# Optimization experiments

Hardware: AMD Instinct MI355X
Metric: run time of the kernel (lower is better)

Reference implementation:

```python
import jax, jax.numpy as jnp
import numpy as np

B, S, T, E, D = 16, 2048, 1024, 256, 256  # batch, src_len, tgt_len, enc_size, dec_size


def setup_inputs() -> dict:
    key = jax.random.key(0)
    k1, k2, k3, k4, k5 = jax.random.split(key, 5)
    enc_states = jax.random.normal(k1, (B, S, E), dtype=jnp.float32)
    dec_states = jax.random.normal(k2, (B, T, D), dtype=jnp.float32)
    # valid-prefix mask: each row has at least one valid (True) source position
    lengths = jax.random.randint(k3, (B,), 1, S + 1)
    src_mask = jnp.arange(S)[None, :] < lengths[:, None]  # (B, S) bool
    # Dense layer weights (no bias). Glorot-ish scale.
    W_enc = jax.random.normal(k4, (E, D), dtype=jnp.float32) / np.sqrt(E)
    W_fin = jax.random.normal(k5, (E + D, D), dtype=jnp.float32) / np.sqrt(E + D)
    return {"enc_states": enc_states, "dec_states": dec_states,
            "src_mask": src_mask, "W_enc": W_enc, "W_fin": W_fin}


def reference(enc_states, dec_states, src_mask, W_enc, W_fin):
    # enc_trnsfrmr: (B,S,E) @ (E,D) -> (B,S,D)
    enc_proj = jnp.einsum('bse,ed->bsd', enc_states, W_enc)
    # attention scores: batch_dot(dec_states, enc_proj^T) -> (B,T,S)
    scores = jnp.einsum('btd,bsd->bts', dec_states, enc_proj)
    scores = jnp.where(src_mask[:, None, :], scores, -jnp.inf)
    wts = jax.nn.softmax(scores, axis=-1)  # (B,T,S)
    # broadcast-multiply + reduce_sum == weighted sum over src positions
    context = jnp.einsum('bts,bse->bte', wts, enc_states)  # (B,T,E)
    cat = jnp.concatenate([context, dec_states], axis=-1)  # (B,T,E+D)
    return jnp.tanh(jnp.einsum('btf,fd->btd', cat, W_fin))  # (B,T,D)
```

## Files before the change

### kernel.cpp

```cpp
#include <hip/hip_runtime.h>
#include <math.h>
#include <stdint.h>

#define NB 16
#define NS 2048
#define NT 1024
#define NE 256
#define ND 256
#define NM (NB * NT)

typedef short sh8 __attribute__((ext_vector_type(8)));
typedef float f4v __attribute__((ext_vector_type(4)));

static __device__ __forceinline__ float bf2f(unsigned short u) {
    union { unsigned int i; float f; } v;
    v.i = ((unsigned int)u) << 16;
    return v.f;
}
static __device__ __forceinline__ unsigned short f2bf(float f) {
    union { unsigned int i; float f; } v;
    v.f = f;
    unsigned int x = v.i;
    x += 0x7FFFu + ((x >> 16) & 1u);
    return (unsigned short)(x >> 16);
}
static __device__ __forceinline__ float4 load4(const void* p, int isbf, long idx) {
    if (isbf) {
        const unsigned short* h = (const unsigned short*)p + idx;
        ushort4 u = *(const ushort4*)h;
        return make_float4(bf2f(u.x), bf2f(u.y), bf2f(u.z), bf2f(u.w));
    }
    const float* f = (const float*)p + idx;
    return *(const float4*)f;
}
static __device__ __forceinline__ int mvalid(const void* m, int kind, int b, int s) {
    long idx = (long)b * NS + s;
    switch (kind) {
        case 0:  return ((const unsigned char*)m)[idx] != 0;
        case 1:  return ((const int*)m)[idx] != 0;
        case 2:  return ((const unsigned short*)m)[idx] != 0;
        default: return ((const unsigned int*)m)[idx] != 0;
    }
}

__global__ void k_detect(const void* __restrict__ enc_raw,
                         const void* __restrict__ mask_raw,
                         int* __restrict__ flags) {
    __shared__ int cnt;
    if (threadIdx.x == 0) cnt = 0;
    __syncthreads();
    const unsigned short* h = (const unsigned short*)enc_raw;
    int local = 0;
    for (int i = threadIdx.x; i < 4096; i += 256) {
        int ex = (h[i] >> 7) & 0xFF;
        if (ex >= 97 && ex <= 157) local++;
    }
    atomicAdd(&cnt, local);
    __syncthreads();
    if (threadIdx.x == 0) {
        int isbf = (cnt >= 3700) ? 1 : 0;
        const unsigned char* mb = (const unsigned char*)mask_raw;
        int kind;
        if (mb[1] == 0x3F)                       kind = 2;
        else if (mb[3] == 0x3F && mb[1] == 0)    kind = 3;
        else if (mb[1] == 1)                     kind = 0;
        else if (mb[4] == 1 || mb[8] == 1)       kind = 1;
        else                                     kind = (mb[NS] == 1) ? 0 : 1;
        flags[0] = isbf;
        flags[1] = kind;
    }
}

__global__ __launch_bounds__(256) void k_split_e(const void* __restrict__ enc,
                                                 const int* __restrict__ flags,
                                                 unsigned short* __restrict__ eh,
                                                 unsigned short* __restrict__ el) {
    const int isbf = flags[0];
    const long i = ((long)blockIdx.x * 256 + threadIdx.x) * 8;
    if (isbf) {
        sh8 v = *(const sh8*)((const unsigned short*)enc + i);
        *(sh8*)(eh + i) = v;
    } else {
        const float* f = (const float*)enc + i;
        sh8 hv, lv;
#pragma unroll
        for (int j = 0; j < 8; ++j) {
            float x = f[j];
            unsigned short h = f2bf(x);
            hv[j] = (short)h;
            lv[j] = (short)f2bf(x - bf2f(h));
        }
        *(sh8*)(eh + i) = hv;
        *(sh8*)(el + i) = lv;
    }
}

__global__ __launch_bounds__(256) void k_q(const void* __restrict__ dec,
                                           const void* __restrict__ Wenc,
                                           const int* __restrict__ flags,
                                           unsigned short* __restrict__ qh,
                                           unsigned short* __restrict__ ql) {
    const int isbf = flags[0];
    const int tid = threadIdx.x;
    const int tx = tid & 15, ty = tid >> 4;
    const int m0 = blockIdx.x * 64, n0 = blockIdx.y * 64;
    __shared__ float As[16][68];
    __shared__ float Bs[16][68];
    float acc[4][4] = {};
    const int lrow = tid >> 2;
    const int lk4  = (tid & 3) << 2;
    for (int kt = 0; kt < ND; kt += 16) {
        float4 av = load4(dec,  isbf, (long)(m0 + lrow) * ND + kt + lk4);
        float4 bv = load4(Wenc, isbf, (long)(n0 + lrow) * ND + kt + lk4);
        As[lk4 + 0][lrow] = av.x; As[lk4 + 1][lrow] = av.y;
        As[lk4 + 2][lrow] = av.z; As[lk4 + 3][lrow] = av.w;
        Bs[lk4 + 0][lrow] = bv.x; Bs[lk4 + 1][lrow] = bv.y;
        Bs[lk4 + 2][lrow] = bv.z; Bs[lk4 + 3][lrow] = bv.w;
        __syncthreads();
#pragma unroll
        for (int k = 0; k < 16; ++k) {
            float4 a = *(const float4*)&As[k][ty << 2];
            float4 b = *(const float4*)&Bs[k][tx << 2];
            acc[0][0] = fmaf(a.x, b.x, acc[0][0]); acc[0][1] = fmaf(a.x, b.y, acc[0][1]);
            acc[0][2] = fmaf(a.x, b.z, acc[0][2]); acc[0][3] = fmaf(a.x, b.w, acc[0][3]);
            acc[1][0] = fmaf(a.y, b.x, acc[1][0]); acc[1][1] = fmaf(a.y, b.y, acc[1][1]);
            acc[1][2] = fmaf(a.y, b.z, acc[1][2]); acc[1][3] = fmaf(a.y, b.w, acc[1][3]);
            acc[2][0] = fmaf(a.z, b.x, acc[2][0]); acc[2][1] = fmaf(a.z, b.y, acc[2][1]);
            acc[2][2] = fmaf(a.z, b.z, acc[2][2]); acc[2][3] = fmaf(a.z, b.w, acc[2][3]);
            acc[3][0] = fmaf(a.w, b.x, acc[3][0]); acc[3][1] = fmaf(a.w, b.y, acc[3][1]);
            acc[3][2] = fmaf(a.w, b.z, acc[3][2]); acc[3][3] = fmaf(a.w, b.w, acc[3][3]);
        }
        __syncthreads();
    }
#pragma unroll
    for (int i = 0; i < 4; ++i) {
        long base = (long)(m0 + (ty << 2) + i) * NE + n0 + (tx << 2);
        ushort4 hv, lv;
        {
            float f0 = acc[i][0]; unsigned short h = f2bf(f0); hv.x = h; lv.x = f2bf(f0 - bf2f(h));
            float f1 = acc[i][1]; h = f2bf(f1); hv.y = h; lv.y = f2bf(f1 - bf2f(h));
            float f2 = acc[i][2]; h = f2bf(f2); hv.z = h; lv.z = f2bf(f2 - bf2f(h));
            float f3 = acc[i][3]; h = f2bf(f3); hv.w = h; lv.w = f2bf(f3 - bf2f(h));
        }
        *(ushort4*)&qh[base] = hv;
        *(ushort4*)&ql[base] = lv;
    }
}

__global__ __launch_bounds__(256, 2) void k_attn(
    const unsigned short* __restrict__ qh, const unsigned short* __restrict__ ql,
    const unsigned short* __restrict__ eh, const unsigned short* __restrict__ el,
    const void* __restrict__ mask, const int* __restrict__ flags,
    float* __restrict__ ctx, float* __restrict__ Mp, float* __restrict__ Lp)
{
    const int isbf  = flags[0];
    const int mkind = flags[1];
    const int b  = blockIdx.y;
    const int t0 = blockIdx.x * 32;
    const int part = blockIdx.z, nparts = gridDim.z;
    const int tid  = threadIdx.x;
    const int lane = tid & 63;
    const int wid  = tid >> 6;
    const int th = wid & 1;
    const int sh = wid >> 1;
    const int lr = lane & 15;
    const int lg = lane >> 4;

    __shared__ __align__(16) unsigned short EHR[32][264];
    __shared__ __align__(16) unsigned short ELR[32][264];
    __shared__ __align__(16) unsigned short VT[2][256][40];
    __shared__ __align__(16) float PBs[32][36];
    __shared__ float hm[2][32];
    __shared__ float hs[2][32];
    __shared__ int s_len;

    if (tid == 0) s_len = 0;
    __syncthreads();
    {
        int c = 0;
#pragma unroll
        for (int j = 0; j < 8; ++j) c += mvalid(mask, mkind, b, tid * 8 + j);
        atomicAdd(&s_len, c);
    }
    __syncthreads();
    const int len  = s_len;
    const int s_lo = part * (NS / nparts);
    const int s_hi = min(s_lo + NS / nparts, len);
    const int ntiles = (s_hi > s_lo) ? ((s_hi - s_lo + 31) >> 5) : 0;
    const long mrow = (long)part * NM + (long)b * NT + t0;
    if (ntiles == 0) {
        if (nparts > 1 && tid < 32) { Mp[mrow + tid] = -INFINITY; Lp[mrow + tid] = 0.f; }
        return;
    }

    sh8 qhf[8], qlf[8];
    {
        const unsigned short* qp  = qh + ((long)b * NT + t0 + th * 16 + lr) * NE + lg * 8;
        const unsigned short* qp2 = ql + ((long)b * NT + t0 + th * 16 + lr) * NE + lg * 8;
#pragma unroll
        for (int k8 = 0; k8 < 8; ++k8) {
            qhf[k8] = *(const sh8*)(qp  + k8 * 32);
            qlf[k8] = *(const sh8*)(qp2 + k8 * 32);
        }
    }

    f4v O[8];
#pragma unroll
    for (int et = 0; et < 8; ++et) O[et] = (f4v){0.f, 0.f, 0.f, 0.f};
    float Mreg4[4], L4[4], MregP = -INFINITY;
#pragma unroll
    for (int r = 0; r < 4; ++r) { Mreg4[r] = -INFINITY; L4[r] = 0.f; }

    const int ss = tid >> 3;
    const int ee = (tid & 7) * 8;
    const int swzw = ((tid & 7) & 3) << 3;

    sh8 rh[4], rl[4];
    {
        const unsigned short* eg = eh + ((long)b * NS + s_lo + ss) * NE;
#pragma unroll
        for (int c = 0; c < 4; ++c) rh[c] = *(const sh8*)(eg + ee + c * 64);
        if (!isbf) {
            const unsigned short* eg2 = el + ((long)b * NS + s_lo + ss) * NE;
#pragma unroll
            for (int c = 0; c < 4; ++c) rl[c] = *(const sh8*)(eg2 + ee + c * 64);
        }
#pragma unroll
        for (int c = 0; c < 4; ++c) {
            const int e0 = ee + c * 64;
            *(sh8*)&EHR[ss][e0] = rh[c];
            if (!isbf) *(sh8*)&ELR[ss][e0] = rl[c];
            const int cs = ss ^ swzw;
#pragma unroll
            for (int j = 0; j < 8; ++j) VT[0][e0 + j][cs] = (unsigned short)rh[c][j];
        }
    }
    int cur = 0;

    for (int it = 0; it < ntiles; ++it) {
        const int s0 = s_lo + it * 32;
        __syncthreads();
        f4v cacc = (f4v){0.f, 0.f, 0.f, 0.f};
        {
            const unsigned short* ep = &EHR[sh * 16 + lr][lg * 8];
            const unsigned short* lp = &ELR[sh * 16 + lr][lg * 8];
            if (isbf) {
#pragma unroll
                for (int k8 = 0; k8 < 8; ++k8) {
                    sh8 ea = *(const sh8*)(ep + k8 * 32);
                    cacc = __builtin_amdgcn_mfma_f32_16x16x32_bf16(ea, qhf[k8], cacc, 0, 0, 0);
                    cacc = __builtin_amdgcn_mfma_f32_16x16x32_bf16(ea, qlf[k8], cacc, 0, 0, 0);
                }
            } else {
#pragma unroll
                for (int k8 = 0; k8 < 8; ++k8) {
                    sh8 ea = *(const sh8*)(ep + k8 * 32);
                    sh8 eb = *(const sh8*)(lp + k8 * 32);
                    cacc = __builtin_amdgcn_mfma_f32_16x16x32_bf16(ea, qhf[k8], cacc, 0, 0, 0);
                    cacc = __builtin_amdgcn_mfma_f32_16x16x32_bf16(ea, qlf[k8], cacc, 0, 0, 0);
                    cacc = __builtin_amdgcn_mfma_f32_16x16x32_bf16(eb, qhf[k8], cacc, 0, 0, 0);
                }
            }
        }
        float sc[4];
#pragma unroll
        for (int r = 0; r < 4; ++r) {
            int sl = sh * 16 + lg * 4 + r;
            sc[r] = (s0 + sl < len) ? cacc[r] : -INFINITY;
        }
        float m4 = fmaxf(fmaxf(sc[0], sc[1]), fmaxf(sc[2], sc[3]));
        m4 = fmaxf(m4, __shfl_xor(m4, 16));
        m4 = fmaxf(m4, __shfl_xor(m4, 32));
        float p[4], ps = 0.f;
#pragma unroll
        for (int r = 0; r < 4; ++r) {
            p[r] = (sc[r] == -INFINITY) ? 0.f : __expf(sc[r] - m4);
            ps += p[r];
        }
        ps += __shfl_xor(ps, 16);
        ps += __shfl_xor(ps, 32);
        if (lane < 16) { hm[sh][th * 16 + lane] = m4; hs[sh][th * 16 + lane] = ps; }
        *(float4*)&PBs[th * 16 + lr][sh * 16 + lg * 4] = make_float4(p[0], p[1], p[2], p[3]);
        __syncthreads();
        float f0, f1, al[4];
        {
            const int tP = th * 16 + lr;
            float h0 = hm[0][tP], h1 = hm[1][tP];
            float Mn = fmaxf(MregP, fmaxf(h0, h1));
            f0 = __expf(h0 - Mn);
            f1 = __expf(h1 - Mn);
            MregP = Mn;
        }
#pragma unroll
        for (int r = 0; r < 4; ++r) {
            const int t4 = th * 16 + lg * 4 + r;
            float g0 = hm[0][t4], g1 = hm[1][t4];
            float Mn = fmaxf(Mreg4[r], fmaxf(g0, g1));
            al[r] = __expf(Mreg4[r] - Mn);
            L4[r] = L4[r] * al[r] + hs[0][t4] * __expf(g0 - Mn) + hs[1][t4] * __expf(g1 - Mn);
            Mreg4[r] = Mn;
        }
        const int more = (it + 1 < ntiles);
        if (more) {
            const unsigned short* eg = eh + ((long)b * NS + s0 + 32 + ss) * NE;
#pragma unroll
            for (int c = 0; c < 4; ++c) rh[c] = *(const sh8*)(eg + ee + c * 64);
            if (!isbf) {
                const unsigned short* eg2 = el + ((long)b * NS + s0 + 32 + ss) * NE;
#pragma unroll
                for (int c = 0; c < 4; ++c) rl[c] = *(const sh8*)(eg2 + ee + c * 64);
            }
        }
        {
            const float fsc = (lg < 2) ? f0 : f1;
            f4v pA = *(const f4v*)&PBs[th * 16 + lr][lg * 8];
            f4v pB = *(const f4v*)&PBs[th * 16 + lr][lg * 8 + 4];
            sh8 pf;
#pragma unroll
            for (int j = 0; j < 4; ++j) {
                pf[j]     = (short)f2bf(pA[j] * fsc);
                pf[4 + j] = (short)f2bf(pB[j] * fsc);
            }
            f4v alv = (f4v){al[0], al[1], al[2], al[3]};
#pragma unroll
            for (int et = 0; et < 8; ++et) O[et] *= alv;
#pragma unroll
            for (int et = 0; et < 8; ++et) {
                const int row = sh * 128 + et * 16 + lr;
                sh8 vf = *(const sh8*)&VT[cur][row][(lg ^ ((row >> 3) & 3)) * 8];
                O[et] = __builtin_amdgcn_mfma_f32_16x16x32_bf16(pf, vf, O[et], 0, 0, 0);
            }
        }
        if (more) {
#pragma unroll
            for (int c = 0; c < 4; ++c) {
                const int e0 = ee + c * 64;
                *(sh8*)&EHR[ss][e0] = rh[c];
                if (!isbf) *(sh8*)&ELR[ss][e0] = rl[c];
                const int cs = ss ^ swzw;
#pragma unroll
                for (int j = 0; j < 8; ++j) VT[cur ^ 1][e0 + j][cs] = (unsigned short)rh[c][j];
            }
            cur ^= 1;
        }
    }
    if (nparts == 1) {
        f4v inv;
#pragma unroll
        for (int r = 0; r < 4; ++r) inv[r] = 1.0f / L4[r];
#pragma unroll
        for (int et = 0; et < 8; ++et) {
            f4v ov = O[et] * inv;
            long rbase = ((long)b * NT + t0 + th * 16 + lg * 4) * NE + sh * 128 + et * 16 + lr;
#pragma unroll
            for (int r = 0; r < 4; ++r)
                ctx[rbase + (long)r * NE] = ov[r];
        }
    } else {
        float* op = ctx + (long)part * NM * NE;
#pragma unroll
        for (int et = 0; et < 8; ++et) {
            long rbase = ((long)b * NT + t0 + th * 16 + lg * 4) * NE + sh * 128 + et * 16 + lr;
#pragma unroll
            for (int r = 0; r < 4; ++r)
                op[rbase + (long)r * NE] = O[et][r];
        }
        if (sh == 0 && lr == 0) {
#pragma unroll
            for (int r = 0; r < 4; ++r) {
                Mp[mrow + th * 16 + lg * 4 + r] = Mreg4[r];
                Lp[mrow + th * 16 + lg * 4 + r] = L4[r];
            }
        }
    }
}

__global__ __launch_bounds__(256) void k_comb(float* __restrict__ ctx,
                                              const float* __restrict__ Mp,
                                              const float* __restrict__ Lp,
                                              int nparts) {
    const long m = (long)blockIdx.x * 8 + (threadIdx.x >> 5);
    const int  e0 = (threadIdx.x & 31) * 8;
    float Mv[4], Lv[4];
    float M = -INFINITY;
    for (int p = 0; p < nparts; ++p) {
        Mv[p] = Mp[(long)p * NM + m];
        Lv[p] = Lp[(long)p * NM + m];
        if (Lv[p] > 0.f) M = fmaxf(M, Mv[p]);
    }
    float L = 0.f, w[4];
    for (int p = 0; p < nparts; ++p) {
        w[p] = (Lv[p] > 0.f) ? __expf(Mv[p] - M) : 0.f;
        L += Lv[p] * w[p];
    }
    float o[8] = {};
    for (int p = 0; p < nparts; ++p) {
        if (w[p] > 0.f) {
            const float* src = ctx + (long)p * NM * NE + m * NE + e0;
            f4v a = *(const f4v*)src;
            f4v c = *(const f4v*)(src + 4);
#pragma unroll
            for (int j = 0; j < 4; ++j) { o[j] += a[j] * w[p]; o[4 + j] += c[j] * w[p]; }
        }
    }
    const float inv = 1.0f / L;
    float* dst = ctx + m * NE + e0;
    f4v r0, r1;
#pragma unroll
    for (int j = 0; j < 4; ++j) { r0[j] = o[j] * inv; r1[j] = o[4 + j] * inv; }
    *(f4v*)dst = r0;
    *(f4v*)(dst + 4) = r1;
}

__global__ __launch_bounds__(256) void k_final(const float* __restrict__ ctx,
                                               const void* __restrict__ dec,
                                               const void* __restrict__ Wfin,
                                               const int* __restrict__ flags,
                                               void* __restrict__ out) {
    const int isbf = flags[0];
    const int tid = threadIdx.x;
    const int tx = tid & 15, ty = tid >> 4;
    const int m0 = blockIdx.x * 64, n0 = blockIdx.y * 64;
    __shared__ float As[16][68];
    __shared__ float Bs[16][68];
    float acc[4][4] = {};
    const int lrow = tid >> 2;
    const int lk4  = (tid & 3) << 2;
    const int lkb  = tid >> 4;
    const int ln4  = (tid & 15) << 2;
    for (int kt = 0; kt < NE + ND; kt += 16) {
        float4 av;
        if (kt < NE) {
            av = *(const float4*)&ctx[(long)(m0 + lrow) * NE + kt + lk4];
        } else {
            av = load4(dec, isbf, (long)(m0 + lrow) * ND + (kt - NE) + lk4);
        }
        float4 bv = load4(Wfin, isbf, (long)(kt + lkb) * ND + n0 + ln4);
        As[lk4 + 0][lrow] = av.x; As[lk4 + 1][lrow] = av.y;
        As[lk4 + 2][lrow] = av.z; As[lk4 + 3][lrow] = av.w;
        *(float4*)&Bs[lkb][ln4] = bv;
        __syncthreads();
#pragma unroll
        for (int k = 0; k < 16; ++k) {
            float4 a = *(const float4*)&As[k][ty << 2];
            float4 b = *(const float4*)&Bs[k][tx << 2];
            acc[0][0] = fmaf(a.x, b.x, acc[0][0]); acc[0][1] = fmaf(a.x, b.y, acc[0][1]);
            acc[0][2] = fmaf(a.x, b.z, acc[0][2]); acc[0][3] = fmaf(a.x, b.w, acc[0][3]);
            acc[1][0] = fmaf(a.y, b.x, acc[1][0]); acc[1][1] = fmaf(a.y, b.y, acc[1][1]);
            acc[1][2] = fmaf(a.y, b.z, acc[1][2]); acc[1][3] = fmaf(a.y, b.w, acc[1][3]);
            acc[2][0] = fmaf(a.z, b.x, acc[2][0]); acc[2][1] = fmaf(a.z, b.y, acc[2][1]);
            acc[2][2] = fmaf(a.z, b.z, acc[2][2]); acc[2][3] = fmaf(a.z, b.w, acc[2][3]);
            acc[3][0] = fmaf(a.w, b.x, acc[3][0]); acc[3][1] = fmaf(a.w, b.y, acc[3][1]);
            acc[3][2] = fmaf(a.w, b.z, acc[3][2]); acc[3][3] = fmaf(a.w, b.w, acc[3][3]);
        }
        __syncthreads();
    }
    if (isbf) {
        unsigned short* o = (unsigned short*)out;
#pragma unroll
        for (int i = 0; i < 4; ++i) {
            long base = (long)(m0 + (ty << 2) + i) * ND + n0 + (tx << 2);
            ushort4 r;
            r.x = f2bf(tanhf(acc[i][0])); r.y = f2bf(tanhf(acc[i][1]));
            r.z = f2bf(tanhf(acc[i][2])); r.w = f2bf(tanhf(acc[i][3]));
            *(ushort4*)&o[base] = r;
        }
    } else {
        float* o = (float*)out;
#pragma unroll
        for (int i = 0; i < 4; ++i) {
            long base = (long)(m0 + (ty << 2) + i) * ND + n0 + (tx << 2);
            float4 r = make_float4(tanhf(acc[i][0]), tanhf(acc[i][1]),
                                   tanhf(acc[i][2]), tanhf(acc[i][3]));
            *(float4*)&o[base] = r;
        }
    }
}

extern "C" void kernel_launch(void* const* d_in, const int* in_sizes, int n_in,
                              void* d_out, int out_size, void* d_ws, size_t ws_size,
                              hipStream_t stream) {
    const void* enc  = d_in[0];
    const void* dec  = d_in[1];
    const void* mask = d_in[2];
    const void* Wenc = d_in[3];
    const void* Wfin = d_in[4];

    unsigned short* ehb = (unsigned short*)d_ws;
    unsigned short* elb = ehb + (size_t)NB * NS * NE;
    unsigned short* qhb = elb + (size_t)NB * NS * NE;
    unsigned short* qlb = qhb + (size_t)NM * NE;
    const size_t fixed = ((size_t)NB * NS * NE * 2 + (size_t)NM * NE * 2) * 2;

    int parts = 1;
    for (int p = 4; p >= 1; p >>= 1) {
        size_t need = fixed + (size_t)p * NM * NE * 4 + (size_t)p * NM * 8 + 256;
        if (ws_size >= need) { parts = p; break; }
    }
    float* ctx  = (float*)(qlb + (size_t)NM * NE);
    float* Mpb  = ctx + (size_t)parts * NM * NE;
    float* Lpb  = Mpb + (size_t)parts * NM;
    int*   flags = (int*)(Lpb + (size_t)parts * NM);

    k_detect<<<1, 256, 0, stream>>>(enc, mask, flags);
    k_split_e<<<(NB * NS * NE) / (256 * 8), 256, 0, stream>>>(enc, flags, ehb, elb);
    k_q<<<dim3(NM / 64, NE / 64), 256, 0, stream>>>(dec, Wenc, flags, qhb, qlb);
    k_attn<<<dim3(NT / 32, NB, parts), 256, 0, stream>>>(qhb, qlb, ehb, elb, mask, flags,
                                                         ctx, Mpb, Lpb);
    if (parts > 1)
        k_comb<<<NM / 8, 256, 0, stream>>>(ctx, Mpb, Lpb, parts);
    k_final<<<dim3(NM / 64, ND / 64), 256, 0, stream>>>(ctx, dec, Wfin, flags, d_out);
}
```

Before: 315.7 us.

## Move query and final projections to split-bf16 MFMA GEMMs

Replaces the FP32 SIMT tiled GEMMs for the query projection and the final concatenated projection with MFMA kernels using hi/lo bf16 splitting (three products) to keep near-FP32 accuracy. Adds split kernels for dec, W_enc and a transposed W_fin. The attention and combine kernels now emit context as hi/lo bf16, reusing the query buffers, so the final GEMM reads MFMA-ready operands. This trades extra preprocessing launches and memory traffic for much higher matrix throughput, and aliasing the q buffers as outputs requires dropping restrict.

```diff
diff --git a/kernel.cpp b/kernel.cpp
--- a/kernel.cpp
+++ b/kernel.cpp
@@ -8,6 +8,7 @@
 #define NE 256
 #define ND 256
 #define NM (NB * NT)
+#define KF (NE + ND)
 
 typedef short sh8 __attribute__((ext_vector_type(8)));
 typedef float f4v __attribute__((ext_vector_type(4)));
@@ -71,17 +72,17 @@
     }
 }
 
-__global__ __launch_bounds__(256) void k_split_e(const void* __restrict__ enc,
-                                                 const int* __restrict__ flags,
-                                                 unsigned short* __restrict__ eh,
-                                                 unsigned short* __restrict__ el) {
+__global__ __launch_bounds__(256) void k_split(const void* __restrict__ src,
+                                               const int* __restrict__ flags,
+                                               unsigned short* __restrict__ hh,
+                                               unsigned short* __restrict__ ll) {
     const int isbf = flags[0];
     const long i = ((long)blockIdx.x * 256 + threadIdx.x) * 8;
     if (isbf) {
-        sh8 v = *(const sh8*)((const unsigned short*)enc + i);
-        *(sh8*)(eh + i) = v;
+        sh8 v = *(const sh8*)((const unsigned short*)src + i);
+        *(sh8*)(hh + i) = v;
     } else {
-        const float* f = (const float*)enc + i;
+        const float* f = (const float*)src + i;
         sh8 hv, lv;
 #pragma unroll
         for (int j = 0; j < 8; ++j) {
@@ -90,68 +91,124 @@
             hv[j] = (short)h;
             lv[j] = (short)f2bf(x - bf2f(h));
         }
-        *(sh8*)(eh + i) = hv;
-        *(sh8*)(el + i) = lv;
-    }
-}
-
-__global__ __launch_bounds__(256) void k_q(const void* __restrict__ dec,
-                                           const void* __restrict__ Wenc,
-                                           const int* __restrict__ flags,
-                                           unsigned short* __restrict__ qh,
-                                           unsigned short* __restrict__ ql) {
+        *(sh8*)(hh + i) = hv;
+        *(sh8*)(ll + i) = lv;
+    }
+}
+
+__global__ __launch_bounds__(256) void k_twf(const void* __restrict__ Wfin,
+                                             const int* __restrict__ flags,
+                                             unsigned short* __restrict__ wfh,
+                                             unsigned short* __restrict__ wfl) {
     const int isbf = flags[0];
+    __shared__ float T[64][68];
+    const int f0 = blockIdx.x * 64, n0 = blockIdx.y * 64;
     const int tid = threadIdx.x;
-    const int tx = tid & 15, ty = tid >> 4;
-    const int m0 = blockIdx.x * 64, n0 = blockIdx.y * 64;
-    __shared__ float As[16][68];
-    __shared__ float Bs[16][68];
-    float acc[4][4] = {};
-    const int lrow = tid >> 2;
-    const int lk4  = (tid & 3) << 2;
-    for (int kt = 0; kt < ND; kt += 16) {
-        float4 av = load4(dec,  isbf, (long)(m0 + lrow) * ND + kt + lk4);
-        float4 bv = load4(Wenc, isbf, (long)(n0 + lrow) * ND + kt + lk4);
-        As[lk4 + 0][lrow] = av.x; As[lk4 + 1][lrow] = av.y;
-        As[lk4 + 2][lrow] = av.z; As[lk4 + 3][lrow] = av.w;
-        Bs[lk4 + 0][lrow] = bv.x; Bs[lk4 + 1][lrow] = bv.y;
-        Bs[lk4 + 2][lrow] = bv.z; Bs[lk4 + 3][lrow] = bv.w;
-        __syncthreads();
-#pragma unroll
-        for (int k = 0; k < 16; ++k) {
-            float4 a = *(const float4*)&As[k][ty << 2];
-            float4 b = *(const float4*)&Bs[k][tx << 2];
-            acc[0][0] = fmaf(a.x, b.x, acc[0][0]); acc[0][1] = fmaf(a.x, b.y, acc[0][1]);
-            acc[0][2] = fmaf(a.x, b.z, acc[0][2]); acc[0][3] = fmaf(a.x, b.w, acc[0][3]);
-            acc[1][0] = fmaf(a.y, b.x, acc[1][0]); acc[1][1] = fmaf(a.y, b.y, acc[1][1]);
-            acc[1][2] = fmaf(a.y, b.z, acc[1][2]); acc[1][3] = fmaf(a.y, b.w, acc[1][3]);
-            acc[2][0] = fmaf(a.z, b.x, acc[2][0]); acc[2][1] = fmaf(a.z, b.y, acc[2][1]);
-            acc[2][2] = fmaf(a.z, b.z, acc[2][2]); acc[2][3] = fmaf(a.z, b.w, acc[2][3]);
-            acc[3][0] = fmaf(a.w, b.x, acc[3][0]); acc[3][1] = fmaf(a.w, b.y, acc[3][1]);
-            acc[3][2] = fmaf(a.w, b.z, acc[3][2]); acc[3][3] = fmaf(a.w, b.w, acc[3][3]);
-        }
-        __syncthreads();
-    }
 #pragma unroll
     for (int i = 0; i < 4; ++i) {
-        long base = (long)(m0 + (ty << 2) + i) * NE + n0 + (tx << 2);
+        int idx = tid + i * 256;
+        int r = idx >> 4, c4 = (idx & 15) << 2;
+        float4 v = load4(Wfin, isbf, (long)(f0 + r) * ND + n0 + c4);
+        T[r][c4] = v.x; T[r][c4 + 1] = v.y; T[r][c4 + 2] = v.z; T[r][c4 + 3] = v.w;
+    }
+    __syncthreads();
+#pragma unroll
+    for (int i = 0; i < 4; ++i) {
+        int idx = tid + i * 256;
+        int n = idx >> 4, f4 = (idx & 15) << 2;
         ushort4 hv, lv;
-        {
-            float f0 = acc[i][0]; unsigned short h = f2bf(f0); hv.x = h; lv.x = f2bf(f0 - bf2f(h));
-            float f1 = acc[i][1]; h = f2bf(f1); hv.y = h; lv.y = f2bf(f1 - bf2f(h));
-            float f2 = acc[i][2]; h = f2bf(f2); hv.z = h; lv.z = f2bf(f2 - bf2f(h));
-            float f3 = acc[i][3]; h = f2bf(f3); hv.w = h; lv.w = f2bf(f3 - bf2f(h));
-        }
-        *(ushort4*)&qh[base] = hv;
-        *(ushort4*)&ql[base] = lv;
-    }
+        float x;
+        x = T[f4 + 0][n]; hv.x = f2bf(x); lv.x = f2bf(x - bf2f(hv.x));
+        x = T[f4 + 1][n]; hv.y = f2bf(x); lv.y = f2bf(x - bf2f(hv.y));
+        x = T[f4 + 2][n]; hv.z = f2bf(x); lv.z = f2bf(x - bf2f(hv.z));
+        x = T[f4 + 3][n]; hv.w = f2bf(x); lv.w = f2bf(x - bf2f(hv.w));
+        long base = (long)(n0 + n) * KF + f0 + f4;
+        *(ushort4*)&wfh[base] = hv;
+        *(ushort4*)&wfl[base] = lv;
+    }
+}
+
+__global__ __launch_bounds__(256) void k_q_m(const unsigned short* __restrict__ dh,
+                                             const unsigned short* __restrict__ dl,
+                                             const unsigned short* __restrict__ wh,
+                                             const unsigned short* __restrict__ wl,
+                                             const int* __restrict__ flags,
+                                             unsigned short* __restrict__ qh,
+                                             unsigned short* __restrict__ ql) {
+    const int isbf = flags[0];
+    const int lane = threadIdx.x & 63, wid = threadIdx.x >> 6;
+    const int lr = lane & 15, lg = lane >> 4;
+    const long m0 = (long)blockIdx.x * 64 + (wid & 1) * 32;
+    const int  n0 = blockIdx.y * 64 + (wid >> 1) * 32;
+    const unsigned short* Ah = dh + (m0 + lr) * ND + lg * 8;
+    const unsigned short* Al = dl + (m0 + lr) * ND + lg * 8;
+    const unsigned short* Bh = wh + (long)(n0 + lr) * ND + lg * 8;
+    const unsigned short* Bl = wl + (long)(n0 + lr) * ND + lg * 8;
+    f4v acc[2][2];
+#pragma unroll
+    for (int i = 0; i < 2; ++i)
+#pragma unroll
+        for (int j = 0; j < 2; ++j) acc[i][j] = (f4v){0.f, 0.f, 0.f, 0.f};
+    if (isbf) {
+#pragma unroll
+        for (int k8 = 0; k8 < 8; ++k8) {
+            const int ko = k8 * 32;
+            sh8 a0 = *(const sh8*)(Ah + ko);
+            sh8 a1 = *(const sh8*)(Ah + 16 * ND + ko);
+            sh8 b0 = *(const sh8*)(Bh + ko);
+            sh8 b1 = *(const sh8*)(Bh + 16 * ND + ko);
+            acc[0][0] = __builtin_amdgcn_mfma_f32_16x16x32_bf16(a0, b0, acc[0][0], 0, 0, 0);
+            acc[0][1] = __builtin_amdgcn_mfma_f32_16x16x32_bf16(a0, b1, acc[0][1], 0, 0, 0);
+            acc[1][0] = __builtin_amdgcn_mfma_f32_16x16x32_bf16(a1, b0, acc[1][0], 0, 0, 0);
+            acc[1][1] = __builtin_amdgcn_mfma_f32_16x16x32_bf16(a1, b1, acc[1][1], 0, 0, 0);
+        }
+    } else {
+#pragma unroll
+        for (int k8 = 0; k8 < 8; ++k8) {
+            const int ko = k8 * 32;
+            sh8 a0 = *(const sh8*)(Ah + ko);
+            sh8 a1 = *(const sh8*)(Ah + 16 * ND + ko);
+            sh8 b0 = *(const sh8*)(Bh + ko);
+            sh8 b1 = *(const sh8*)(Bh + 16 * ND + ko);
+            sh8 la0 = *(const sh8*)(Al + ko);
+            sh8 la1 = *(const sh8*)(Al + 16 * ND + ko);
+            sh8 lb0 = *(const sh8*)(Bl + ko);
+            sh8 lb1 = *(const sh8*)(Bl + 16 * ND + ko);
+            acc[0][0] = __builtin_amdgcn_mfma_f32_16x16x32_bf16(a0, b0, acc[0][0], 0, 0, 0);
+            acc[0][0] = __builtin_amdgcn_mfma_f32_16x16x32_bf16(la0, b0, acc[0][0], 0, 0, 0);
+            acc[0][0] = __builtin_amdgcn_mfma_f32_16x16x32_bf16(a0, lb0, acc[0][0], 0, 0, 0);
+            acc[0][1] = __builtin_amdgcn_mfma_f32_16x16x32_bf16(a0, b1, acc[0][1], 0, 0, 0);
+            acc[0][1] = __builtin_amdgcn_mfma_f32_16x16x32_bf16(la0, b1, acc[0][1], 0, 0, 0);
+            acc[0][1] = __builtin_amdgcn_mfma_f32_16x16x32_bf16(a0, lb1, acc[0][1], 0, 0, 0);
+            acc[1][0] = __builtin_amdgcn_mfma_f32_16x16x32_bf16(a1, b0, acc[1][0], 0, 0, 0);
+            acc[1][0] = __builtin_amdgcn_mfma_f32_16x16x32_bf16(la1, b0, acc[1][0], 0, 0, 0);
+            acc[1][0] = __builtin_amdgcn_mfma_f32_16x16x32_bf16(a1, lb0, acc[1][0], 0, 0, 0);
+            acc[1][1] = __builtin_amdgcn_mfma_f32_16x16x32_bf16(a1, b1, acc[1][1], 0, 0, 0);
+            acc[1][1] = __builtin_amdgcn_mfma_f32_16x16x32_bf16(la1, b1, acc[1][1], 0, 0, 0);
+            acc[1][1] = __builtin_amdgcn_mfma_f32_16x16x32_bf16(a1, lb1, acc[1][1], 0, 0, 0);
+        }
+    }
+#pragma unroll
+    for (int mi = 0; mi < 2; ++mi)
+#pragma unroll
+        for (int r = 0; r < 4; ++r) {
+            long rowb = (m0 + mi * 16 + lg * 4 + r) * NE + n0 + lr;
+#pragma unroll
+            for (int ni = 0; ni < 2; ++ni) {
+                float v = acc[mi][ni][r];
+                unsigned short h = f2bf(v);
+                qh[rowb + ni * 16] = h;
+                ql[rowb + ni * 16] = f2bf(v - bf2f(h));
+            }
+        }
 }
 
 __global__ __launch_bounds__(256, 2) void k_attn(
-    const unsigned short* __restrict__ qh, const unsigned short* __restrict__ ql,
+    const unsigned short* qh, const unsigned short* ql,
     const unsigned short* __restrict__ eh, const unsigned short* __restrict__ el,
     const void* __restrict__ mask, const int* __restrict__ flags,
-    float* __restrict__ ctx, float* __restrict__ Mp, float* __restrict__ Lp)
+    unsigned short* ch, unsigned short* cl,
+    float* __restrict__ pctx, float* __restrict__ Mp, float* __restrict__ Lp)
 {
     const int isbf  = flags[0];
     const int mkind = flags[1];
@@ -353,11 +410,15 @@
             f4v ov = O[et] * inv;
             long rbase = ((long)b * NT + t0 + th * 16 + lg * 4) * NE + sh * 128 + et * 16 + lr;
 #pragma unroll
-            for (int r = 0; r < 4; ++r)
-                ctx[rbase + (long)r * NE] = ov[r];
+            for (int r = 0; r < 4; ++r) {
+                float v = ov[r];
+                unsigned short h = f2bf(v);
+                ch[rbase + (long)r * NE] = h;
+                cl[rbase + (long)r * NE] = f2bf(v - bf2f(h));
+            }
         }
     } else {
-        float* op = ctx + (long)part * NM * NE;
+        float* op = pctx + (long)part * NM * NE;
 #pragma unroll
         for (int et = 0; et < 8; ++et) {
             long rbase = ((long)b * NT + t0 + th * 16 + lg * 4) * NE + sh * 128 + et * 16 + lr;
@@ -375,10 +436,12 @@
     }
 }
 
-__global__ __launch_bounds__(256) void k_comb(float* __restrict__ ctx,
+__global__ __launch_bounds__(256) void k_comb(const float* __restrict__ pctx,
                                               const float* __restrict__ Mp,
                                               const float* __restrict__ Lp,
-                                              int nparts) {
+                                              int nparts,
+                                              unsigned short* __restrict__ ch,
+                                              unsigned short* __restrict__ cl) {
     const long m = (long)blockIdx.x * 8 + (threadIdx.x >> 5);
     const int  e0 = (threadIdx.x & 31) * 8;
     float Mv[4], Lv[4];
@@ -396,7 +459,7 @@
     float o[8] = {};
     for (int p = 0; p < nparts; ++p) {
         if (w[p] > 0.f) {
-            const float* src = ctx + (long)p * NM * NE + m * NE + e0;
+            const float* src = pctx + (long)p * NM * NE + m * NE + e0;
             f4v a = *(const f4v*)src;
             f4v c = *(const f4v*)(src + 4);
 #pragma unroll
@@ -404,76 +467,126 @@
         }
     }
     const float inv = 1.0f / L;
-    float* dst = ctx + m * NE + e0;
-    f4v r0, r1;
-#pragma unroll
-    for (int j = 0; j < 4; ++j) { r0[j] = o[j] * inv; r1[j] = o[4 + j] * inv; }
-    *(f4v*)dst = r0;
-    *(f4v*)(dst + 4) = r1;
-}
-
-__global__ __launch_bounds__(256) void k_final(const float* __restrict__ ctx,
-                                               const void* __restrict__ dec,
-                                               const void* __restrict__ Wfin,
+    unsigned short hv[8], lv[8];
+#pragma unroll
+    for (int j = 0; j < 8; ++j) {
+        float v = o[j] * inv;
+        unsigned short h = f2bf(v);
+        hv[j] = h;
+        lv[j] = f2bf(v - bf2f(h));
+    }
+    long base = m * NE + e0;
+    *(ushort4*)&ch[base]     = *(ushort4*)&hv[0];
+    *(ushort4*)&ch[base + 4] = *(ushort4*)&hv[4];
+    *(ushort4*)&cl[base]     = *(ushort4*)&lv[0];
+    *(ushort4*)&cl[base + 4] = *(ushort4*)&lv[4];
+}
+
+__global__ __launch_bounds__(256) void k_fin_m(const unsigned short* __restrict__ ch,
+                                               const unsigned short* __restrict__ cl,
+                                               const unsigned short* __restrict__ dh,
+                                               const unsigned short* __restrict__ dl,
+                                               const unsigned short* __restrict__ wh,
+                                               const unsigned short* __restrict__ wl,
                                                const int* __restrict__ flags,
                                                void* __restrict__ out) {
     const int isbf = flags[0];
-    const int tid = threadIdx.x;
-    const int tx = tid & 15, ty = tid >> 4;
-    const int m0 = blockIdx.x * 64, n0 = blockIdx.y * 64;
-    __shared__ float As[16][68];
-    __shared__ float Bs[16][68];
-    float acc[4][4] = {};
-    const int lrow = tid >> 2;
-    const int lk4  = (tid & 3) << 2;
-    const int lkb  = tid >> 4;
-    const int ln4  = (tid & 15) << 2;
-    for (int kt = 0; kt < NE + ND; kt += 16) {
-        float4 av;
-        if (kt < NE) {
-            av = *(const float4*)&ctx[(long)(m0 + lrow) * NE + kt + lk4];
-        } else {
-            av = load4(dec, isbf, (long)(m0 + lrow) * ND + (kt - NE) + lk4);
-        }
-        float4 bv = load4(Wfin, isbf, (long)(kt + lkb) * ND + n0 + ln4);
-        As[lk4 + 0][lrow] = av.x; As[lk4 + 1][lrow] = av.y;
-        As[lk4 + 2][lrow] = av.z; As[lk4 + 3][lrow] = av.w;
-        *(float4*)&Bs[lkb][ln4] = bv;
-        __syncthreads();
-#pragma unroll
-        for (int k = 0; k < 16; ++k) {
-            float4 a = *(const float4*)&As[k][ty << 2];
-            float4 b = *(const float4*)&Bs[k][tx << 2];
-            acc[0][0] = fmaf(a.x, b.x, acc[0][0]); acc[0][1] = fmaf(a.x, b.y, acc[0][1]);
-            acc[0][2] = fmaf(a.x, b.z, acc[0][2]); acc[0][3] = fmaf(a.x, b.w, acc[0][3]);
-            acc[1][0] = fmaf(a.y, b.x, acc[1][0]); acc[1][1] = fmaf(a.y, b.y, acc[1][1]);
-            acc[1][2] = fmaf(a.y, b.z, acc[1][2]); acc[1][3] = fmaf(a.y, b.w, acc[1][3]);
-            acc[2][0] = fmaf(a.z, b.x, acc[2][0]); acc[2][1] = fmaf(a.z, b.y, acc[2][1]);
-            acc[2][2] = fmaf(a.z, b.z, acc[2][2]); acc[2][3] = fmaf(a.z, b.w, acc[2][3]);
-            acc[3][0] = fmaf(a.w, b.x, acc[3][0]); acc[3][1] = fmaf(a.w, b.y, acc[3][1]);
-            acc[3][2] = fmaf(a.w, b.z, acc[3][2]); acc[3][3] = fmaf(a.w, b.w, acc[3][3]);
-        }
-        __syncthreads();
+    const int lane = threadIdx.x & 63, wid = threadIdx.x >> 6;
+    const int lr = lane & 15, lg = lane >> 4;
+    const long m0 = (long)blockIdx.x * 64 + (wid & 1) * 32;
+    const int  n0 = blockIdx.y * 64 + (wid >> 1) * 32;
+    const unsigned short* Bh = wh + (long)(n0 + lr) * KF + lg * 8;
+    const unsigned short* Bl = wl + (long)(n0 + lr) * KF + lg * 8;
+    f4v acc[2][2];
+#pragma unroll
+    for (int i = 0; i < 2; ++i)
+#pragma unroll
+        for (int j = 0; j < 2; ++j) acc[i][j] = (f4v){0.f, 0.f, 0.f, 0.f};
+
+    {
+        const unsigned short* Ah = ch + (m0 + lr) * NE + lg * 8;
+        const unsigned short* Al = cl + (m0 + lr) * NE + lg * 8;
+#pragma unroll
+        for (int k8 = 0; k8 < 8; ++k8) {
+            const int ko = k8 * 32;
+            sh8 a0 = *(const sh8*)(Ah + ko);
+            sh8 a1 = *(const sh8*)(Ah + 16 * NE + ko);
+            sh8 la0 = *(const sh8*)(Al + ko);
+            sh8 la1 = *(const sh8*)(Al + 16 * NE + ko);
+            sh8 b0 = *(const sh8*)(Bh + ko);
+            sh8 b1 = *(const sh8*)(Bh + 16 * KF + ko);
+            acc[0][0] = __builtin_amdgcn_mfma_f32_16x16x32_bf16(a0, b0, acc[0][0], 0, 0, 0);
+            acc[0][0] = __builtin_amdgcn_mfma_f32_16x16x32_bf16(la0, b0, acc[0][0], 0, 0, 0);
+            acc[0][1] = __builtin_amdgcn_mfma_f32_16x16x32_bf16(a0, b1, acc[0][1], 0, 0, 0);
+            acc[0][1] = __builtin_amdgcn_mfma_f32_16x16x32_bf16(la0, b1, acc[0][1], 0, 0, 0);
+            acc[1][0] = __builtin_amdgcn_mfma_f32_16x16x32_bf16(a1, b0, acc[1][0], 0, 0, 0);
+            acc[1][0] = __builtin_amdgcn_mfma_f32_16x16x32_bf16(la1, b0, acc[1][0], 0, 0, 0);
+            acc[1][1] = __builtin_amdgcn_mfma_f32_16x16x32_bf16(a1, b1, acc[1][1], 0, 0, 0);
+            acc[1][1] = __builtin_amdgcn_mfma_f32_16x16x32_bf16(la1, b1, acc[1][1], 0, 0, 0);
+            if (!isbf) {
+                sh8 lb0 = *(const sh8*)(Bl + ko);
+                sh8 lb1 = *(const sh8*)(Bl + 16 * KF + ko);
+                acc[0][0] = __builtin_amdgcn_mfma_f32_16x16x32_bf16(a0, lb0, acc[0][0], 0, 0, 0);
+                acc[0][1] = __builtin_amdgcn_mfma_f32_16x16x32_bf16(a0, lb1, acc[0][1], 0, 0, 0);
+                acc[1][0] = __builtin_amdgcn_mfma_f32_16x16x32_bf16(a1, lb0, acc[1][0], 0, 0, 0);
+                acc[1][1] = __builtin_amdgcn_mfma_f32_16x16x32_bf16(a1, lb1, acc[1][1], 0, 0, 0);
+            }
+        }
+    }
+    {
+        const unsigned short* Ah = dh + (m0 + lr) * ND + lg * 8;
+        const unsigned short* Al = dl + (m0 + lr) * ND + lg * 8;
+        const unsigned short* B2h = Bh + NE;
+        const unsigned short* B2l = Bl + NE;
+#pragma unroll
+        for (int k8 = 0; k8 < 8; ++k8) {
+            const int ko = k8 * 32;
+            sh8 a0 = *(const sh8*)(Ah + ko);
+            sh8 a1 = *(const sh8*)(Ah + 16 * ND + ko);
+            sh8 b0 = *(const sh8*)(B2h + ko);
+            sh8 b1 = *(const sh8*)(B2h + 16 * KF + ko);
+            acc[0][0] = __builtin_amdgcn_mfma_f32_16x16x32_bf16(a0, b0, acc[0][0], 0, 0, 0);
+            acc[0][1] = __builtin_amdgcn_mfma_f32_16x16x32_bf16(a0, b1, acc[0][1], 0, 0, 0);
+            acc[1][0] = __builtin_amdgcn_mfma_f32_16x16x32_bf16(a1, b0, acc[1][0], 0, 0, 0);
+            acc[1][1] = __builtin_amdgcn_mfma_f32_16x16x32_bf16(a1, b1, acc[1][1], 0, 0, 0);
+            if (!isbf) {
+                sh8 la0 = *(const sh8*)(Al + ko);
+                sh8 la1 = *(const sh8*)(Al + 16 * ND + ko);
+                sh8 lb0 = *(const sh8*)(B2l + ko);
+                sh8 lb1 = *(const sh8*)(B2l + 16 * KF + ko);
+                acc[0][0] = __builtin_amdgcn_mfma_f32_16x16x32_bf16(la0, b0, acc[0][0], 0, 0, 0);
+                acc[0][0] = __builtin_amdgcn_mfma_f32_16x16x32_bf16(a0, lb0, acc[0][0], 0, 0, 0);
+                acc[0][1] = __builtin_amdgcn_mfma_f32_16x16x32_bf16(la0, b1, acc[0][1], 0, 0, 0);
+                acc[0][1] = __builtin_amdgcn_mfma_f32_16x16x32_bf16(a0, lb1, acc[0][1], 0, 0, 0);
+                acc[1][0] = __builtin_amdgcn_mfma_f32_16x16x32_bf16(la1, b0, acc[1][0], 0, 0, 0);
+                acc[1][0] = __builtin_amdgcn_mfma_f32_16x16x32_bf16(a1, lb0, acc[1][0], 0, 0, 0);
+                acc[1][1] = __builtin_amdgcn_mfma_f32_16x16x32_bf16(la1, b1, acc[1][1], 0, 0, 0);
+                acc[1][1] = __builtin_amdgcn_mfma_f32_16x16x32_bf16(a1, lb1, acc[1][1], 0, 0, 0);
+            }
+        }
     }
     if (isbf) {
         unsigned short* o = (unsigned short*)out;
 #pragma unroll
-        for (int i = 0; i < 4; ++i) {
-            long base = (long)(m0 + (ty << 2) + i) * ND + n0 + (tx << 2);
-            ushort4 r;
-            r.x = f2bf(tanhf(acc[i][0])); r.y = f2bf(tanhf(acc[i][1]));
-            r.z = f2bf(tanhf(acc[i][2])); r.w = f2bf(tanhf(acc[i][3]));
-            *(ushort4*)&o[base] = r;
-        }
+        for (int mi = 0; mi < 2; ++mi)
+#pragma unroll
+            for (int r = 0; r < 4; ++r) {
+                long rowb = (m0 + mi * 16 + lg * 4 + r) * ND + n0 + lr;
+#pragma unroll
+                for (int ni = 0; ni < 2; ++ni)
+                    o[rowb + ni * 16] = f2bf(tanhf(acc[mi][ni][r]));
+            }
     } else {
         float* o = (float*)out;
 #pragma unroll
-        for (int i = 0; i < 4; ++i) {
-            long base = (long)(m0 + (ty << 2) + i) * ND + n0 + (tx << 2);
-            float4 r = make_float4(tanhf(acc[i][0]), tanhf(acc[i][1]),
-                                   tanhf(acc[i][2]), tanhf(acc[i][3]));
-            *(float4*)&o[base] = r;
-        }
+        for (int mi = 0; mi < 2; ++mi)
+#pragma unroll
+            for (int r = 0; r < 4; ++r) {
+                long rowb = (m0 + mi * 16 + lg * 4 + r) * ND + n0 + lr;
+#pragma unroll
+                for (int ni = 0; ni < 2; ++ni)
+                    o[rowb + ni * 16] = tanhf(acc[mi][ni][r]);
+            }
     }
 }
 
@@ -490,24 +603,35 @@
     unsigned short* elb = ehb + (size_t)NB * NS * NE;
     unsigned short* qhb = elb + (size_t)NB * NS * NE;
     unsigned short* qlb = qhb + (size_t)NM * NE;
-    const size_t fixed = ((size_t)NB * NS * NE * 2 + (size_t)NM * NE * 2) * 2;
-
+    unsigned short* dhb = qlb + (size_t)NM * NE;
+    unsigned short* dlb = dhb + (size_t)NM * ND;
+    unsigned short* weh = dlb + (size_t)NM * ND;
+    unsigned short* wel = weh + (size_t)NE * ND;
+    unsigned short* wfh = wel + (size_t)NE * ND;
+    unsigned short* wfl = wfh + (size_t)KF * ND;
+    unsigned short* wend = wfl + (size_t)KF * ND;
+
+    const size_t fixed = (size_t)((char*)wend - (char*)d_ws);
     int parts = 1;
     for (int p = 4; p >= 1; p >>= 1) {
-        size_t need = fixed + (size_t)p * NM * NE * 4 + (size_t)p * NM * 8 + 256;
+        size_t need = fixed + ((p > 1) ? ((size_t)p * NM * NE * 4 + (size_t)p * NM * 8) : 0) + 256;
         if (ws_size >= need) { parts = p; break; }
     }
-    float* ctx  = (float*)(qlb + (size_t)NM * NE);
-    float* Mpb  = ctx + (size_t)parts * NM * NE;
+    float* pctx = (float*)wend;
+    float* Mpb  = pctx + ((parts > 1) ? (size_t)parts * NM * NE : 0);
     float* Lpb  = Mpb + (size_t)parts * NM;
     int*   flags = (int*)(Lpb + (size_t)parts * NM);
 
     k_detect<<<1, 256, 0, stream>>>(enc, mask, flags);
-    k_split_e<<<(NB * NS * NE) / (256 * 8), 256, 0, stream>>>(enc, flags, ehb, elb);
-    k_q<<<dim3(NM / 64, NE / 64), 256, 0, stream>>>(dec, Wenc, flags, qhb, qlb);
+    k_split<<<(NB * NS * NE) / 2048, 256, 0, stream>>>(enc, flags, ehb, elb);
+    k_split<<<(NM * ND) / 2048, 256, 0, stream>>>(dec, flags, dhb, dlb);
+    k_split<<<(NE * ND) / 2048, 256, 0, stream>>>(Wenc, flags, weh, wel);
+    k_twf<<<dim3(KF / 64, ND / 64), 256, 0, stream>>>(Wfin, flags, wfh, wfl);
+    k_q_m<<<dim3(NM / 64, NE / 64), 256, 0, stream>>>(dhb, dlb, weh, wel, flags, qhb, qlb);
     k_attn<<<dim3(NT / 32, NB, parts), 256, 0, stream>>>(qhb, qlb, ehb, elb, mask, flags,
-                                                         ctx, Mpb, Lpb);
+                                                         qhb, qlb, pctx, Mpb, Lpb);
     if (parts > 1)
-        k_comb<<<NM / 8, 256, 0, stream>>>(ctx, Mpb, Lpb, parts);
-    k_final<<<dim3(NM / 64, ND / 64), 256, 0, stream>>>(ctx, dec, Wfin, flags, d_out);
-}
+        k_comb<<<NM / 8, 256, 0, stream>>>(pctx, Mpb, Lpb, parts, qhb, qlb);
+    k_fin_m<<<dim3(NM / 64, ND / 64), 256, 0, stream>>>(qhb, qlb, dhb, dlb, wfh, wfl,
+                                                        flags, d_out);
+}
```

New measurement: 320.5 us. About the same (+1.5%).
